# Performance work log

Hardware: AMD Instinct MI355X
Metric: run time of the kernel (lower is better)

The kernel has to match this reference:

```python
import jax, jax.numpy as jnp
import numpy as np

H = 8          # num_heads
T = 2          # num_edge_types
NEG_SLOPE = 0.2


def _edge_softmax(scores, dst, num_nodes):
    # softmax over incoming edges of each destination node, per head
    m = jax.ops.segment_max(scores, dst, num_segments=num_nodes)  # [N,H]
    e = jnp.exp(scores - m[dst])                                   # [E,H]
    s = jax.ops.segment_sum(e, dst, num_segments=num_nodes)        # [N,H]
    return e / s[dst]


def setup_inputs() -> dict:
    key = jax.random.key(0)
    ks = jax.random.split(key, 8)
    N, D, E = 50000, 128, 800000
    return {
        "x": jax.random.normal(ks[0], (N, D), dtype=jnp.float32),
        "w_u": jax.random.normal(ks[1], (H * T, D), dtype=jnp.float32) * (1.0 / np.sqrt(D)),
        "b_u": jax.random.normal(ks[2], (H * T,), dtype=jnp.float32) * 0.01,
        "w_v": jax.random.normal(ks[3], (H * T, D), dtype=jnp.float32) * (1.0 / np.sqrt(D)),
        "src_e0": jax.random.randint(ks[4], (E,), 0, N, dtype=jnp.int32),
        "dst_e0": jax.random.randint(ks[5], (E,), 0, N, dtype=jnp.int32),
        "src_e1": jax.random.randint(ks[6], (E,), 0, N, dtype=jnp.int32),
        "dst_e1": jax.random.randint(ks[7], (E,), 0, N, dtype=jnp.int32),
    }


def reference(x, w_u, b_u, w_v, src_e0, dst_e0, src_e1, dst_e1):
    N, D = x.shape
    head_dim = D // H
    scores_u = x @ w_u.T + b_u   # [N, H*T]
    scores_v = x @ w_v.T         # [N, H*T]
    xh = x.reshape(N, head_dim, H)  # matches torch reshape(-1, head_dim, num_heads)
    outs = [x]  # sep=True
    for t, (src, dst) in enumerate([(src_e0, dst_e0), (src_e1, dst_e1)]):
        u = scores_u[:, t * H:(t + 1) * H]
        v = scores_v[:, t * H:(t + 1) * H]
        s = u[src] + v[dst]                         # u_add_v -> [E,H]
        s = jnp.where(s >= 0, s, NEG_SLOPE * s)     # LeakyReLU(0.2)
        p = _edge_softmax(s, dst, N)                # [E,H]
        msg = xh[src] * p[:, None, :]               # u_mul_e -> [E,head_dim,H]
        agg = jax.ops.segment_sum(msg, dst, num_segments=N)  # [N,head_dim,H]
        outs.append(agg.reshape(N, D))
    return jnp.concatenate(outs, axis=-1)  # [N, D*(1+T)]
```

## Files before the change

### kernel.cpp

```cpp
#include <hip/hip_runtime.h>

#define NEG_SLOPE 0.2f
#define RSHIFT 5
#define RW     32
#define MAXNR  1600
#define CHUNKP 8192

__device__ __forceinline__ ushort f2bf(float f) {
    union { float f; unsigned u; } c; c.f = f;
    unsigned u = c.u;
    return (ushort)((u + 0x7fffu + ((u >> 16) & 1u)) >> 16);
}
__device__ __forceinline__ float bflo(unsigned u) { return __uint_as_float(u << 16); }
__device__ __forceinline__ float bfhi(unsigned u) { return __uint_as_float(u & 0xffff0000u); }

__global__ __launch_bounds__(256) void mega_kernel(
    const float* __restrict__ x, const float* __restrict__ wu,
    const float* __restrict__ bu, const float* __restrict__ wv,
    const int* __restrict__ s0, const int* __restrict__ d0,
    const int* __restrict__ s1, const int* __restrict__ d1,
    float* __restrict__ out, ushort* __restrict__ xbf,
    float* __restrict__ su, float* __restrict__ sv,
    int* __restrict__ gcur, unsigned* __restrict__ pairs,
    int N, int E, int nr, int cap, int scoreBlocks, int ppset)
{
    __shared__ __align__(16) float smemf[32 * 129 + 16 * 132];
    int* smi = (int*)smemf;
    float* wlds = smemf;
    float* xtile = smemf + 32 * 129;
    int tid = threadIdx.x;
    int bid = blockIdx.x;

    if (bid < 2 * ppset) {
        int pb = bid;
        int t = pb / ppset, c = pb % ppset;
        const int* ss = t ? s1 : s0;
        const int* dd = t ? d1 : d0;
        int beg = c * CHUNKP, end = min(E, beg + CHUNKP);
        int* lcnt = smi; int* gb = smi + MAXNR; int* lrun = smi + 2 * MAXNR;
        for (int i = tid; i < nr; i += 256) lcnt[i] = 0;
        __syncthreads();
        for (int e = beg + tid; e < end; e += 256)
            atomicAdd(&lcnt[dd[e] >> RSHIFT], 1);
        __syncthreads();
        for (int i = tid; i < nr; i += 256) {
            gb[i] = atomicAdd(&gcur[t * nr + i], lcnt[i]);
            lrun[i] = 0;
        }
        __syncthreads();
        unsigned* pt = pairs + (size_t)t * nr * cap;
        for (int e = beg + tid; e < end; e += 256) {
            int dst = dd[e], src = ss[e];
            int rr = dst >> RSHIFT;
            int pos = atomicAdd(&lrun[rr], 1);
            pt[(size_t)rr * cap + gb[rr] + pos] = ((unsigned)dst << 16) | (unsigned)src;
        }
        return;
    }
    int nb = bid - 2 * ppset;
    int base = nb * 16;
    for (int i = tid; i < 4096; i += 256) {
        int o = i >> 7, k = i & 127;
        wlds[o * 129 + k] = (o < 16) ? wu[i] : wv[i - 2048];
    }
    for (int i2 = tid; i2 < 512; i2 += 256) {
        int I = nb * 512 + i2;
        int nl = i2 >> 5, q = i2 & 31;
        int n = base + nl;
        float4 v = make_float4(0.f, 0.f, 0.f, 0.f);
        if (n < N) {
            v = ((const float4*)x)[I];
            ((float4*)out)[(size_t)n * 96 + q] = v;
            ushort4 b;
            b.x = f2bf(v.x); b.y = f2bf(v.y); b.z = f2bf(v.z); b.w = f2bf(v.w);
            *(ushort4*)(xbf + (size_t)I * 4) = b;
        }
        ((float4*)(xtile + nl * 132))[q] = v;
    }
    __syncthreads();
    int o = tid & 15;
    int nl = tid >> 4;
    int n = base + nl;
    if (n >= N) return;
    const float4* xr4 = (const float4*)(xtile + nl * 132);
    const float* wur = wlds + o * 129;
    const float* wvr = wlds + (16 + o) * 129;
    float au = 0.f, av = 0.f;
#pragma unroll
    for (int kk = 0; kk < 32; ++kk) {
        float4 xv = xr4[kk];
        int k = kk * 4;
        au = fmaf(xv.x, wur[k],     au);  av = fmaf(xv.x, wvr[k],     av);
        au = fmaf(xv.y, wur[k + 1], au);  av = fmaf(xv.y, wvr[k + 1], av);
        au = fmaf(xv.z, wur[k + 2], au);  av = fmaf(xv.z, wvr[k + 2], av);
        au = fmaf(xv.w, wur[k + 3], au);  av = fmaf(xv.w, wvr[k + 3], av);
    }
    float resu = au + bu[o];
    float resv = av;
    size_t toff = (o < 8) ? 0 : (size_t)N * 8;
    int ho = o & 7;
    su[toff + (size_t)n * 8 + ho] = resu;
    sv[toff + (size_t)n * 8 + ho] = resv;
}

__global__ __launch_bounds__(256, 8) void buildagg_kernel(
    const ushort* __restrict__ xbf, const float* __restrict__ su,
    const float* __restrict__ sv, const int* __restrict__ gcur,
    const unsigned* __restrict__ pairs, float* __restrict__ out,
    int N, int E, int nr, int cap)
{
    __shared__ ushort srcs[768];
    __shared__ int offl[33];
    __shared__ int cursor[32];
    __shared__ __align__(16) float ev4[4][512];
    int r = blockIdx.x, t = blockIdx.y, tid = threadIdx.x;
    int m = gcur[t * nr + r];
    if (m > cap) m = cap;
    const unsigned* p = pairs + ((size_t)t * nr + r) * cap;
    const float* sut = su + (size_t)t * N * 8;
    const float* svt = sv + (size_t)t * N * 8;

    unsigned* pl = (unsigned*)ev4;
    for (int i = tid; i < m; i += 256)
        pl[i] = p[i];
    if (tid < 32) cursor[tid] = 0;
    __syncthreads();
    for (int i = tid; i < m; i += 256)
        atomicAdd(&cursor[(pl[i] >> 16) & (RW - 1)], 1);
    __syncthreads();
    if (tid < 32) {
        int v = cursor[tid];
        int incl = v;
#pragma unroll
        for (int d = 1; d < 32; d <<= 1) {
            int o = __shfl(incl, tid - d);
            if (tid >= d) incl += o;
        }
        offl[tid + 1] = incl;
        if (tid == 0) offl[0] = 0;
        cursor[tid] = incl - v;
    }
    __syncthreads();
    for (int i = tid; i < m; i += 256) {
        unsigned v = pl[i];
        int pos = atomicAdd(&cursor[(v >> 16) & (RW - 1)], 1);
        srcs[pos] = (ushort)(v & 0xffffu);
    }
    __syncthreads();

    int wid = tid >> 6, lane = tid & 63;
    int g2 = lane >> 4, q16 = lane & 15;
    int j0 = q16 * 8;
    int eg = lane >> 1;
    int hh = (lane & 1) * 4;
    float* ev = ev4[wid];
    for (int ln = wid; ln < RW; ln += 4) {
        int n = (r << RSHIFT) + ln;
        if (n >= N) break;
        int beg = offl[ln], end = offl[ln + 1];
        float4 vh4 = *(const float4*)(svt + (size_t)n * 8 + hh);
        float a0 = 0.f, a1 = 0.f, a2 = 0.f, a3 = 0.f;
        float a4 = 0.f, a5 = 0.f, a6 = 0.f, a7 = 0.f;
        float4 l4 = make_float4(0.f, 0.f, 0.f, 0.f);
        for (int cbeg = beg; cbeg < end; cbeg += 64) {
            int cnt = min(end - cbeg, 64);
            int gmax = (cnt + 31) >> 5;
            for (int g = 0; g < gmax; ++g) {
                int e = g * 32 + eg;
                bool valid = e < cnt;
                int sidx = srcs[cbeg + (valid ? e : 0)];
                float4 fu = *(const float4*)(sut + (size_t)sidx * 8 + hh);
                float sx = fu.x + vh4.x; sx = (sx >= 0.f) ? sx : NEG_SLOPE * sx;
                float sy = fu.y + vh4.y; sy = (sy >= 0.f) ? sy : NEG_SLOPE * sy;
                float sz = fu.z + vh4.z; sz = (sz >= 0.f) ? sz : NEG_SLOPE * sz;
                float sw = fu.w + vh4.w; sw = (sw >= 0.f) ? sw : NEG_SLOPE * sw;
                float4 ee;
                ee.x = valid ? __expf(sx) : 0.f;
                ee.y = valid ? __expf(sy) : 0.f;
                ee.z = valid ? __expf(sz) : 0.f;
                ee.w = valid ? __expf(sw) : 0.f;
                l4.x += ee.x; l4.y += ee.y; l4.z += ee.z; l4.w += ee.w;
                *(float4*)(ev + e * 8 + hh) = ee;
            }
            int quads = (cnt + 3) >> 2;
            for (int i4 = 0; i4 < quads; i4 += 2) {
                int e0 = (i4 << 2) + g2, e1 = e0 + 4;
                int sA = srcs[cbeg + ((e0 < cnt) ? e0 : 0)];
                int sB = srcs[cbeg + ((e1 < cnt) ? e1 : 0)];
                uint4 uA = *(const uint4*)(xbf + (size_t)sA * 128 + j0);
                uint4 uB = *(const uint4*)(xbf + (size_t)sB * 128 + j0);
                float4 pA0 = *(const float4*)(ev + e0 * 8);
                float4 pA1 = *(const float4*)(ev + e0 * 8 + 4);
                float4 pB0 = *(const float4*)(ev + e1 * 8);
                float4 pB1 = *(const float4*)(ev + e1 * 8 + 4);
                a0 = fmaf(bflo(uA.x), pA0.x, a0);
                a1 = fmaf(bfhi(uA.x), pA0.y, a1);
                a2 = fmaf(bflo(uA.y), pA0.z, a2);
                a3 = fmaf(bfhi(uA.y), pA0.w, a3);
                a4 = fmaf(bflo(uA.z), pA1.x, a4);
                a5 = fmaf(bfhi(uA.z), pA1.y, a5);
                a6 = fmaf(bflo(uA.w), pA1.z, a6);
                a7 = fmaf(bfhi(uA.w), pA1.w, a7);
                a0 = fmaf(bflo(uB.x), pB0.x, a0);
                a1 = fmaf(bfhi(uB.x), pB0.y, a1);
                a2 = fmaf(bflo(uB.y), pB0.z, a2);
                a3 = fmaf(bfhi(uB.y), pB0.w, a3);
                a4 = fmaf(bflo(uB.z), pB1.x, a4);
                a5 = fmaf(bfhi(uB.z), pB1.y, a5);
                a6 = fmaf(bflo(uB.w), pB1.z, a6);
                a7 = fmaf(bfhi(uB.w), pB1.w, a7);
            }
        }
        l4.x += __shfl_xor(l4.x, 2);  l4.y += __shfl_xor(l4.y, 2);
        l4.z += __shfl_xor(l4.z, 2);  l4.w += __shfl_xor(l4.w, 2);
        l4.x += __shfl_xor(l4.x, 4);  l4.y += __shfl_xor(l4.y, 4);
        l4.z += __shfl_xor(l4.z, 4);  l4.w += __shfl_xor(l4.w, 4);
        l4.x += __shfl_xor(l4.x, 8);  l4.y += __shfl_xor(l4.y, 8);
        l4.z += __shfl_xor(l4.z, 8);  l4.w += __shfl_xor(l4.w, 8);
        l4.x += __shfl_xor(l4.x, 16); l4.y += __shfl_xor(l4.y, 16);
        l4.z += __shfl_xor(l4.z, 16); l4.w += __shfl_xor(l4.w, 16);
        l4.x += __shfl_xor(l4.x, 32); l4.y += __shfl_xor(l4.y, 32);
        l4.z += __shfl_xor(l4.z, 32); l4.w += __shfl_xor(l4.w, 32);
        float4 invl4;
        invl4.x = (l4.x > 0.f) ? (1.f / l4.x) : 0.f;
        invl4.y = (l4.y > 0.f) ? (1.f / l4.y) : 0.f;
        invl4.z = (l4.z > 0.f) ? (1.f / l4.z) : 0.f;
        invl4.w = (l4.w > 0.f) ? (1.f / l4.w) : 0.f;
        a0 += __shfl_xor(a0, 16); a0 += __shfl_xor(a0, 32);
        a1 += __shfl_xor(a1, 16); a1 += __shfl_xor(a1, 32);
        a2 += __shfl_xor(a2, 16); a2 += __shfl_xor(a2, 32);
        a3 += __shfl_xor(a3, 16); a3 += __shfl_xor(a3, 32);
        a4 += __shfl_xor(a4, 16); a4 += __shfl_xor(a4, 32);
        a5 += __shfl_xor(a5, 16); a5 += __shfl_xor(a5, 32);
        a6 += __shfl_xor(a6, 16); a6 += __shfl_xor(a6, 32);
        a7 += __shfl_xor(a7, 16); a7 += __shfl_xor(a7, 32);
        float ih0 = __shfl(invl4.x, 0);
        float ih1 = __shfl(invl4.y, 0);
        float ih2 = __shfl(invl4.z, 0);
        float ih3 = __shfl(invl4.w, 0);
        float ih4 = __shfl(invl4.x, 1);
        float ih5 = __shfl(invl4.y, 1);
        float ih6 = __shfl(invl4.z, 1);
        float ih7 = __shfl(invl4.w, 1);
        if (g2 == 0) {
            float* op = out + (size_t)n * 384 + 128 + (size_t)t * 128 + j0;
            *(float4*)op       = make_float4(a0 * ih0, a1 * ih1, a2 * ih2, a3 * ih3);
            *(float4*)(op + 4) = make_float4(a4 * ih4, a5 * ih5, a6 * ih6, a7 * ih7);
        }
    }
}

extern "C" void kernel_launch(void* const* d_in, const int* in_sizes, int n_in,
                              void* d_out, int out_size, void* d_ws, size_t ws_size,
                              hipStream_t stream)
{
    const float* x  = (const float*)d_in[0];
    const float* wu = (const float*)d_in[1];
    const float* bu = (const float*)d_in[2];
    const float* wv = (const float*)d_in[3];
    const int* s0 = (const int*)d_in[4];
    const int* d0 = (const int*)d_in[5];
    const int* s1 = (const int*)d_in[6];
    const int* d1 = (const int*)d_in[7];
    float* out = (float*)d_out;
    int N = in_sizes[0] / 128;
    int E = in_sizes[4];

    int nr = ((N - 1) >> RSHIFT) + 1;
    long long mean = (long long)RW * E / N;
    int cap = (int)(mean + mean / 4 + 64);

    char* ws = (char*)d_ws;
    size_t o = 0;
    auto alloc = [&](size_t bytes) -> void* {
        void* p = ws + o;
        o = (o + bytes + 255) & ~(size_t)255;
        return p;
    };
    float* su       = (float*)alloc((size_t)N * 16 * 4);
    float* sv       = (float*)alloc((size_t)N * 16 * 4);
    int* gcur       = (int*)alloc((size_t)2 * nr * 4);
    unsigned* pairs = (unsigned*)alloc((size_t)2 * nr * cap * 4);
    ushort* xbf     = (ushort*)alloc((size_t)N * 128 * 2);

    int scoreBlocks = (N + 15) / 16;
    int ppset       = (E + CHUNKP - 1) / CHUNKP;

    hipMemsetAsync(gcur, 0, (size_t)2 * nr * 4, stream);
    mega_kernel<<<scoreBlocks + 2 * ppset, 256, 0, stream>>>(
        x, wu, bu, wv, s0, d0, s1, d1, out, xbf, su, sv,
        gcur, pairs, N, E, nr, cap, scoreBlocks, ppset);
    buildagg_kernel<<<dim3(nr, 2), 256, 0, stream>>>(
        xbf, su, sv, gcur, pairs, out, N, E, nr, cap);
}
```

Baseline: 243.7 us.

## Software-pipeline edge score computation across nodes with double-buffered LDS

Restructures the per-warp node loop in the aggregation kernel so the next node's source-score gather and exp computation for its first 64 edges are issued while the current node's bf16 feature gather and accumulation run. Edge weights go into double-buffered shared memory, which doubles the LDS scratch from 8 KB to 16 KB per block. The aim is to hide gather latency on the scattered su loads. In exchange the kernel carries more registers and LDS per block, which may reduce occupancy.

Result: slower. 308.6 us (+26.6%).

```diff
diff --git a/kernel.cpp b/kernel.cpp
--- a/kernel.cpp
+++ b/kernel.cpp
@@ -112,7 +112,7 @@
     __shared__ ushort srcs[768];
     __shared__ int offl[33];
     __shared__ int cursor[32];
-    __shared__ __align__(16) float ev4[4][512];
+    __shared__ __align__(16) float ev8[4][2][512];
     int r = blockIdx.x, t = blockIdx.y, tid = threadIdx.x;
     int m = gcur[t * nr + r];
     if (m > cap) m = cap;
@@ -120,7 +120,7 @@
     const float* sut = su + (size_t)t * N * 8;
     const float* svt = sv + (size_t)t * N * 8;
 
-    unsigned* pl = (unsigned*)ev4;
+    unsigned* pl = (unsigned*)ev8;
     for (int i = tid; i < m; i += 256)
         pl[i] = p[i];
     if (tid < 32) cursor[tid] = 0;
@@ -153,46 +153,94 @@
     int j0 = q16 * 8;
     int eg = lane >> 1;
     int hh = (lane & 1) * 4;
-    float* ev = ev4[wid];
-    for (int ln = wid; ln < RW; ln += 4) {
-        int n = (r << RSHIFT) + ln;
-        if (n >= N) break;
-        int beg = offl[ln], end = offl[ln + 1];
-        float4 vh4 = *(const float4*)(svt + (size_t)n * 8 + hh);
+    float* evw = &ev8[wid][0][0];
+
+    bool actC; int begC = 0, cntC = 0, par = 0;
+    float4 l4C = make_float4(0.f, 0.f, 0.f, 0.f);
+    {
+        int n0 = (r << RSHIFT) + wid;
+        actC = (n0 < N);
+        float4 vh0 = make_float4(0.f, 0.f, 0.f, 0.f);
+        float4 fu0 = make_float4(0.f, 0.f, 0.f, 0.f);
+        int c1 = 0;
+        if (actC) {
+            begC = offl[wid];
+            cntC = offl[wid + 1] - begC;
+            c1 = min(cntC, 64);
+            vh0 = *(const float4*)(svt + (size_t)n0 * 8 + hh);
+            int sA = (int)srcs[begC + ((eg < c1) ? eg : 0)];
+            if (c1 == 0) sA = 0;
+            fu0 = *(const float4*)(sut + (size_t)sA * 8 + hh);
+        }
+        if (actC && cntC > 0) {
+            float sx = fu0.x + vh0.x; sx = (sx >= 0.f) ? sx : NEG_SLOPE * sx;
+            float sy = fu0.y + vh0.y; sy = (sy >= 0.f) ? sy : NEG_SLOPE * sy;
+            float sz = fu0.z + vh0.z; sz = (sz >= 0.f) ? sz : NEG_SLOPE * sz;
+            float sw = fu0.w + vh0.w; sw = (sw >= 0.f) ? sw : NEG_SLOPE * sw;
+            bool vA = eg < c1;
+            float4 ee;
+            ee.x = vA ? __expf(sx) : 0.f;
+            ee.y = vA ? __expf(sy) : 0.f;
+            ee.z = vA ? __expf(sz) : 0.f;
+            ee.w = vA ? __expf(sw) : 0.f;
+            l4C = ee;
+            *(float4*)(evw + eg * 8 + hh) = ee;
+            if (c1 > 32) {
+                int e2 = 32 + eg;
+                int s2 = (int)srcs[begC + ((e2 < c1) ? e2 : 0)];
+                float4 fu2 = *(const float4*)(sut + (size_t)s2 * 8 + hh);
+                float tx = fu2.x + vh0.x; tx = (tx >= 0.f) ? tx : NEG_SLOPE * tx;
+                float ty = fu2.y + vh0.y; ty = (ty >= 0.f) ? ty : NEG_SLOPE * ty;
+                float tz = fu2.z + vh0.z; tz = (tz >= 0.f) ? tz : NEG_SLOPE * tz;
+                float tw = fu2.w + vh0.w; tw = (tw >= 0.f) ? tw : NEG_SLOPE * tw;
+                bool vB = e2 < c1;
+                float4 e2e;
+                e2e.x = vB ? __expf(tx) : 0.f;
+                e2e.y = vB ? __expf(ty) : 0.f;
+                e2e.z = vB ? __expf(tz) : 0.f;
+                e2e.w = vB ? __expf(tw) : 0.f;
+                l4C.x += e2e.x; l4C.y += e2e.y; l4C.z += e2e.z; l4C.w += e2e.w;
+                *(float4*)(evw + e2 * 8 + hh) = e2e;
+            }
+        }
+    }
+
+#pragma unroll 1
+    for (int i = 0; i < 8; ++i) {
+        bool lastN = (i == 7);
+        bool actN = false; int begN = 0, cntN = 0;
+        float4 fuAn = make_float4(0.f, 0.f, 0.f, 0.f);
+        float4 vhn  = make_float4(0.f, 0.f, 0.f, 0.f);
+        if (!lastN) {
+            int lnN = wid + 4 * (i + 1);
+            int nN = (r << RSHIFT) + lnN;
+            actN = (nN < N);
+            if (actN) {
+                begN = offl[lnN];
+                cntN = offl[lnN + 1] - begN;
+                int c1 = min(cntN, 64);
+                vhn = *(const float4*)(svt + (size_t)nN * 8 + hh);
+                int sA = (int)srcs[begN + ((eg < c1) ? eg : 0)];
+                if (c1 == 0) sA = 0;
+                fuAn = *(const float4*)(sut + (size_t)sA * 8 + hh);
+            }
+        }
         float a0 = 0.f, a1 = 0.f, a2 = 0.f, a3 = 0.f;
         float a4 = 0.f, a5 = 0.f, a6 = 0.f, a7 = 0.f;
-        float4 l4 = make_float4(0.f, 0.f, 0.f, 0.f);
-        for (int cbeg = beg; cbeg < end; cbeg += 64) {
-            int cnt = min(end - cbeg, 64);
-            int gmax = (cnt + 31) >> 5;
-            for (int g = 0; g < gmax; ++g) {
-                int e = g * 32 + eg;
-                bool valid = e < cnt;
-                int sidx = srcs[cbeg + (valid ? e : 0)];
-                float4 fu = *(const float4*)(sut + (size_t)sidx * 8 + hh);
-                float sx = fu.x + vh4.x; sx = (sx >= 0.f) ? sx : NEG_SLOPE * sx;
-                float sy = fu.y + vh4.y; sy = (sy >= 0.f) ? sy : NEG_SLOPE * sy;
-                float sz = fu.z + vh4.z; sz = (sz >= 0.f) ? sz : NEG_SLOPE * sz;
-                float sw = fu.w + vh4.w; sw = (sw >= 0.f) ? sw : NEG_SLOPE * sw;
-                float4 ee;
-                ee.x = valid ? __expf(sx) : 0.f;
-                ee.y = valid ? __expf(sy) : 0.f;
-                ee.z = valid ? __expf(sz) : 0.f;
-                ee.w = valid ? __expf(sw) : 0.f;
-                l4.x += ee.x; l4.y += ee.y; l4.z += ee.z; l4.w += ee.w;
-                *(float4*)(ev + e * 8 + hh) = ee;
-            }
-            int quads = (cnt + 3) >> 2;
+        float* evc = evw + par * 512;
+        if (actC && cntC > 0) {
+            int c1 = min(cntC, 64);
+            int quads = (c1 + 3) >> 2;
             for (int i4 = 0; i4 < quads; i4 += 2) {
                 int e0 = (i4 << 2) + g2, e1 = e0 + 4;
-                int sA = srcs[cbeg + ((e0 < cnt) ? e0 : 0)];
-                int sB = srcs[cbeg + ((e1 < cnt) ? e1 : 0)];
+                int sA = srcs[begC + ((e0 < c1) ? e0 : 0)];
+                int sB = srcs[begC + ((e1 < c1) ? e1 : 0)];
                 uint4 uA = *(const uint4*)(xbf + (size_t)sA * 128 + j0);
                 uint4 uB = *(const uint4*)(xbf + (size_t)sB * 128 + j0);
-                float4 pA0 = *(const float4*)(ev + e0 * 8);
-                float4 pA1 = *(const float4*)(ev + e0 * 8 + 4);
-                float4 pB0 = *(const float4*)(ev + e1 * 8);
-                float4 pB1 = *(const float4*)(ev + e1 * 8 + 4);
+                float4 pA0 = *(const float4*)(evc + e0 * 8);
+                float4 pA1 = *(const float4*)(evc + e0 * 8 + 4);
+                float4 pB0 = *(const float4*)(evc + e1 * 8);
+                float4 pB1 = *(const float4*)(evc + e1 * 8 + 4);
                 a0 = fmaf(bflo(uA.x), pA0.x, a0);
                 a1 = fmaf(bfhi(uA.x), pA0.y, a1);
                 a2 = fmaf(bflo(uA.y), pA0.z, a2);
@@ -210,43 +258,133 @@
                 a6 = fmaf(bflo(uB.w), pB1.z, a6);
                 a7 = fmaf(bfhi(uB.w), pB1.w, a7);
             }
-        }
-        l4.x += __shfl_xor(l4.x, 2);  l4.y += __shfl_xor(l4.y, 2);
-        l4.z += __shfl_xor(l4.z, 2);  l4.w += __shfl_xor(l4.w, 2);
-        l4.x += __shfl_xor(l4.x, 4);  l4.y += __shfl_xor(l4.y, 4);
-        l4.z += __shfl_xor(l4.z, 4);  l4.w += __shfl_xor(l4.w, 4);
-        l4.x += __shfl_xor(l4.x, 8);  l4.y += __shfl_xor(l4.y, 8);
-        l4.z += __shfl_xor(l4.z, 8);  l4.w += __shfl_xor(l4.w, 8);
-        l4.x += __shfl_xor(l4.x, 16); l4.y += __shfl_xor(l4.y, 16);
-        l4.z += __shfl_xor(l4.z, 16); l4.w += __shfl_xor(l4.w, 16);
-        l4.x += __shfl_xor(l4.x, 32); l4.y += __shfl_xor(l4.y, 32);
-        l4.z += __shfl_xor(l4.z, 32); l4.w += __shfl_xor(l4.w, 32);
-        float4 invl4;
-        invl4.x = (l4.x > 0.f) ? (1.f / l4.x) : 0.f;
-        invl4.y = (l4.y > 0.f) ? (1.f / l4.y) : 0.f;
-        invl4.z = (l4.z > 0.f) ? (1.f / l4.z) : 0.f;
-        invl4.w = (l4.w > 0.f) ? (1.f / l4.w) : 0.f;
-        a0 += __shfl_xor(a0, 16); a0 += __shfl_xor(a0, 32);
-        a1 += __shfl_xor(a1, 16); a1 += __shfl_xor(a1, 32);
-        a2 += __shfl_xor(a2, 16); a2 += __shfl_xor(a2, 32);
-        a3 += __shfl_xor(a3, 16); a3 += __shfl_xor(a3, 32);
-        a4 += __shfl_xor(a4, 16); a4 += __shfl_xor(a4, 32);
-        a5 += __shfl_xor(a5, 16); a5 += __shfl_xor(a5, 32);
-        a6 += __shfl_xor(a6, 16); a6 += __shfl_xor(a6, 32);
-        a7 += __shfl_xor(a7, 16); a7 += __shfl_xor(a7, 32);
-        float ih0 = __shfl(invl4.x, 0);
-        float ih1 = __shfl(invl4.y, 0);
-        float ih2 = __shfl(invl4.z, 0);
-        float ih3 = __shfl(invl4.w, 0);
-        float ih4 = __shfl(invl4.x, 1);
-        float ih5 = __shfl(invl4.y, 1);
-        float ih6 = __shfl(invl4.z, 1);
-        float ih7 = __shfl(invl4.w, 1);
-        if (g2 == 0) {
-            float* op = out + (size_t)n * 384 + 128 + (size_t)t * 128 + j0;
-            *(float4*)op       = make_float4(a0 * ih0, a1 * ih1, a2 * ih2, a3 * ih3);
-            *(float4*)(op + 4) = make_float4(a4 * ih4, a5 * ih5, a6 * ih6, a7 * ih7);
-        }
+            for (int cbeg = begC + 64; cbeg < begC + cntC; cbeg += 64) {
+                int cnt = min(begC + cntC - cbeg, 64);
+                int gmax = (cnt + 31) >> 5;
+                for (int g = 0; g < gmax; ++g) {
+                    int e = g * 32 + eg;
+                    bool valid = e < cnt;
+                    int sidx = srcs[cbeg + (valid ? e : 0)];
+                    float4 fu = *(const float4*)(sut + (size_t)sidx * 8 + hh);
+                    float4 vh4 = *(const float4*)(svt +
+                        (size_t)((r << RSHIFT) + wid + 4 * i) * 8 + hh);
+                    float sx = fu.x + vh4.x; sx = (sx >= 0.f) ? sx : NEG_SLOPE * sx;
+                    float sy = fu.y + vh4.y; sy = (sy >= 0.f) ? sy : NEG_SLOPE * sy;
+                    float sz = fu.z + vh4.z; sz = (sz >= 0.f) ? sz : NEG_SLOPE * sz;
+                    float sw = fu.w + vh4.w; sw = (sw >= 0.f) ? sw : NEG_SLOPE * sw;
+                    float4 ee;
+                    ee.x = valid ? __expf(sx) : 0.f;
+                    ee.y = valid ? __expf(sy) : 0.f;
+                    ee.z = valid ? __expf(sz) : 0.f;
+                    ee.w = valid ? __expf(sw) : 0.f;
+                    l4C.x += ee.x; l4C.y += ee.y; l4C.z += ee.z; l4C.w += ee.w;
+                    *(float4*)(evc + e * 8 + hh) = ee;
+                }
+                int q2 = (cnt + 3) >> 2;
+                for (int i4 = 0; i4 < q2; i4 += 2) {
+                    int e0 = (i4 << 2) + g2, e1 = e0 + 4;
+                    int sA = srcs[cbeg + ((e0 < cnt) ? e0 : 0)];
+                    int sB = srcs[cbeg + ((e1 < cnt) ? e1 : 0)];
+                    uint4 uA = *(const uint4*)(xbf + (size_t)sA * 128 + j0);
+                    uint4 uB = *(const uint4*)(xbf + (size_t)sB * 128 + j0);
+                    float4 pA0 = *(const float4*)(evc + e0 * 8);
+                    float4 pA1 = *(const float4*)(evc + e0 * 8 + 4);
+                    float4 pB0 = *(const float4*)(evc + e1 * 8);
+                    float4 pB1 = *(const float4*)(evc + e1 * 8 + 4);
+                    a0 = fmaf(bflo(uA.x), pA0.x, a0);
+                    a1 = fmaf(bfhi(uA.x), pA0.y, a1);
+                    a2 = fmaf(bflo(uA.y), pA0.z, a2);
+                    a3 = fmaf(bfhi(uA.y), pA0.w, a3);
+                    a4 = fmaf(bflo(uA.z), pA1.x, a4);
+                    a5 = fmaf(bfhi(uA.z), pA1.y, a5);
+                    a6 = fmaf(bflo(uA.w), pA1.z, a6);
+                    a7 = fmaf(bfhi(uA.w), pA1.w, a7);
+                    a0 = fmaf(bflo(uB.x), pB0.x, a0);
+                    a1 = fmaf(bfhi(uB.x), pB0.y, a1);
+                    a2 = fmaf(bflo(uB.y), pB0.z, a2);
+                    a3 = fmaf(bfhi(uB.y), pB0.w, a3);
+                    a4 = fmaf(bflo(uB.z), pB1.x, a4);
+                    a5 = fmaf(bfhi(uB.z), pB1.y, a5);
+                    a6 = fmaf(bflo(uB.w), pB1.z, a6);
+                    a7 = fmaf(bfhi(uB.w), pB1.w, a7);
+                }
+            }
+        }
+        if (actC) {
+            float4 l4 = l4C;
+            l4.x += __shfl_xor(l4.x, 2);  l4.y += __shfl_xor(l4.y, 2);
+            l4.z += __shfl_xor(l4.z, 2);  l4.w += __shfl_xor(l4.w, 2);
+            l4.x += __shfl_xor(l4.x, 4);  l4.y += __shfl_xor(l4.y, 4);
+            l4.z += __shfl_xor(l4.z, 4);  l4.w += __shfl_xor(l4.w, 4);
+            l4.x += __shfl_xor(l4.x, 8);  l4.y += __shfl_xor(l4.y, 8);
+            l4.z += __shfl_xor(l4.z, 8);  l4.w += __shfl_xor(l4.w, 8);
+            l4.x += __shfl_xor(l4.x, 16); l4.y += __shfl_xor(l4.y, 16);
+            l4.z += __shfl_xor(l4.z, 16); l4.w += __shfl_xor(l4.w, 16);
+            l4.x += __shfl_xor(l4.x, 32); l4.y += __shfl_xor(l4.y, 32);
+            l4.z += __shfl_xor(l4.z, 32); l4.w += __shfl_xor(l4.w, 32);
+            float4 invl4;
+            invl4.x = (l4.x > 0.f) ? (1.f / l4.x) : 0.f;
+            invl4.y = (l4.y > 0.f) ? (1.f / l4.y) : 0.f;
+            invl4.z = (l4.z > 0.f) ? (1.f / l4.z) : 0.f;
+            invl4.w = (l4.w > 0.f) ? (1.f / l4.w) : 0.f;
+            a0 += __shfl_xor(a0, 16); a0 += __shfl_xor(a0, 32);
+            a1 += __shfl_xor(a1, 16); a1 += __shfl_xor(a1, 32);
+            a2 += __shfl_xor(a2, 16); a2 += __shfl_xor(a2, 32);
+            a3 += __shfl_xor(a3, 16); a3 += __shfl_xor(a3, 32);
+            a4 += __shfl_xor(a4, 16); a4 += __shfl_xor(a4, 32);
+            a5 += __shfl_xor(a5, 16); a5 += __shfl_xor(a5, 32);
+            a6 += __shfl_xor(a6, 16); a6 += __shfl_xor(a6, 32);
+            a7 += __shfl_xor(a7, 16); a7 += __shfl_xor(a7, 32);
+            float ih0 = __shfl(invl4.x, 0);
+            float ih1 = __shfl(invl4.y, 0);
+            float ih2 = __shfl(invl4.z, 0);
+            float ih3 = __shfl(invl4.w, 0);
+            float ih4 = __shfl(invl4.x, 1);
+            float ih5 = __shfl(invl4.y, 1);
+            float ih6 = __shfl(invl4.z, 1);
+            float ih7 = __shfl(invl4.w, 1);
+            if (g2 == 0) {
+                int n = (r << RSHIFT) + wid + 4 * i;
+                float* op = out + (size_t)n * 384 + 128 + (size_t)t * 128 + j0;
+                *(float4*)op       = make_float4(a0 * ih0, a1 * ih1, a2 * ih2, a3 * ih3);
+                *(float4*)(op + 4) = make_float4(a4 * ih4, a5 * ih5, a6 * ih6, a7 * ih7);
+            }
+        }
+        float4 l4n = make_float4(0.f, 0.f, 0.f, 0.f);
+        if (!lastN && actN && cntN > 0) {
+            float* evn = evw + (par ^ 1) * 512;
+            int c1 = min(cntN, 64);
+            float sx = fuAn.x + vhn.x; sx = (sx >= 0.f) ? sx : NEG_SLOPE * sx;
+            float sy = fuAn.y + vhn.y; sy = (sy >= 0.f) ? sy : NEG_SLOPE * sy;
+            float sz = fuAn.z + vhn.z; sz = (sz >= 0.f) ? sz : NEG_SLOPE * sz;
+            float sw = fuAn.w + vhn.w; sw = (sw >= 0.f) ? sw : NEG_SLOPE * sw;
+            bool vA = eg < c1;
+            float4 ee;
+            ee.x = vA ? __expf(sx) : 0.f;
+            ee.y = vA ? __expf(sy) : 0.f;
+            ee.z = vA ? __expf(sz) : 0.f;
+            ee.w = vA ? __expf(sw) : 0.f;
+            l4n = ee;
+            *(float4*)(evn + eg * 8 + hh) = ee;
+            if (c1 > 32) {
+                int e2 = 32 + eg;
+                int s2 = (int)srcs[begN + ((e2 < c1) ? e2 : 0)];
+                float4 fu2 = *(const float4*)(sut + (size_t)s2 * 8 + hh);
+                float tx = fu2.x + vhn.x; tx = (tx >= 0.f) ? tx : NEG_SLOPE * tx;
+                float ty = fu2.y + vhn.y; ty = (ty >= 0.f) ? ty : NEG_SLOPE * ty;
+                float tz = fu2.z + vhn.z; tz = (tz >= 0.f) ? tz : NEG_SLOPE * tz;
+                float tw = fu2.w + vhn.w; tw = (tw >= 0.f) ? tw : NEG_SLOPE * tw;
+                bool vB = e2 < c1;
+                float4 e2e;
+                e2e.x = vB ? __expf(tx) : 0.f;
+                e2e.y = vB ? __expf(ty) : 0.f;
+                e2e.z = vB ? __expf(tz) : 0.f;
+                e2e.w = vB ? __expf(tw) : 0.f;
+                l4n.x += e2e.x; l4n.y += e2e.y; l4n.z += e2e.z; l4n.w += e2e.w;
+                *(float4*)(evn + e2 * 8 + hh) = e2e;
+            }
+        }
+        actC = actN; begC = begN; cntC = cntN; l4C = l4n; par ^= 1;
     }
 }
 
```
